# Kernel optimization log

Hardware: AMD Instinct MI355X
Metric: run time of the kernel (lower is better)

Reference implementation:

```python
import jax, jax.numpy as jnp
import numpy as np

N_NODES = 40000
N_EDGES = 640000
NFEAT = 256
NHID = 128


def setup_inputs() -> dict:
    key = jax.random.key(0)
    k1, k2, k3, k4 = jax.random.split(key, 4)
    x = jax.random.normal(k1, (N_NODES, NFEAT), dtype=jnp.float32)
    edge_index = jax.random.randint(k2, (2, N_EDGES), 0, N_NODES, dtype=jnp.int64)
    edge_weight = jax.random.uniform(k3, (N_EDGES,), dtype=jnp.float32)
    # Glorot-style init for the GraphConvolution weight, zero bias
    W = jax.random.normal(k4, (NFEAT, NHID), dtype=jnp.float32) * (1.0 / np.sqrt(NFEAT))
    b = jnp.zeros((NHID,), dtype=jnp.float32)
    return {"x": x, "edge_index": edge_index, "edge_weight": edge_weight, "W": W, "b": b}


def reference(x, edge_index, edge_weight, W, b):
    # GraphConvolution: support = x @ W ; out = spmm(adj, support) + b ; relu
    support = x @ W                                   # [N, nhid]
    src, dst = edge_index[0], edge_index[1]
    msgs = support[src] * edge_weight[:, None]        # [E, nhid] gathered messages
    agg = jax.ops.segment_sum(msgs, dst, num_segments=N_NODES)  # [N, nhid]
    return jax.nn.relu(agg + b)
```

## Files before the change

### kernel.cpp

```cpp
#include <hip/hip_runtime.h>

#define NNODES 40000
#define NEDGES 640000
#define NFEAT  256
#define NHID   128

#define RSHIFT 7
#define RNODES 128
#define NR     313
#define CAPR   3000
#define PARTB  250
#define EPT    10
#define EPB    2560
#define CAPB   32
#define GEMM_BLOCKS (NNODES / 64)

#define SUP_OFF  0u
#define WT_OFF   10240000u
#define CNT_OFF  10305536u
#define EBIN_OFF 10465536u
#define WS_NEEDED (EBIN_OFF + (size_t)NR * PARTB * CAPB * 8)

typedef float floatx4 __attribute__((ext_vector_type(4)));
typedef __bf16 bf16x8 __attribute__((ext_vector_type(8)));
typedef unsigned short ushort8 __attribute__((ext_vector_type(8)));
union BfFrag { ushort8 s; bf16x8 b; };

__device__ __forceinline__ unsigned short f2bf(float f) {
    unsigned int u = __float_as_uint(f);
    u = (u + 0x7FFFu + ((u >> 16) & 1u)) >> 16;
    return (unsigned short)u;
}

__device__ __forceinline__ float4 bf4(unsigned int lo, unsigned int hi) {
    float4 v;
    v.x = __uint_as_float(lo << 16);
    v.y = __uint_as_float(lo & 0xFFFF0000u);
    v.z = __uint_as_float(hi << 16);
    v.w = __uint_as_float(hi & 0xFFFF0000u);
    return v;
}

__global__ __launch_bounds__(256) void setup_wt(const float* __restrict__ W,
                                                unsigned short* __restrict__ Wt) {
    const int i = blockIdx.x * 256 + threadIdx.x;
    const int h = i >> 8;
    const int k = i & 255;
    Wt[i] = f2bf(W[k * NHID + h]);
}

__global__ __launch_bounds__(256) void gemm_fill(const float* __restrict__ x,
                                                 const unsigned short* __restrict__ Wt,
                                                 unsigned short* __restrict__ support,
                                                 const int* __restrict__ ei,
                                                 const float* __restrict__ ew,
                                                 unsigned short* __restrict__ cnt,
                                                 unsigned long long* __restrict__ ebin) {
    const int tid = threadIdx.x;

    if (blockIdx.x >= GEMM_BLOCKS) {
        __shared__ unsigned int ldscur[320];
        const int pb   = blockIdx.x - GEMM_BLOCKS;
        const int base = pb * EPB + tid;

        for (int i = tid; i < 320; i += 256) ldscur[i] = 0u;
        __syncthreads();

        int src[EPT], dst[EPT];
        float w[EPT];
        #pragma unroll
        for (int j = 0; j < EPT; j++) {
            const int e = base + j * 256;
            src[j] = ei[e];
            dst[j] = ei[NEDGES + e];
            w[j]   = ew[e];
        }
        #pragma unroll
        for (int j = 0; j < EPT; j++) {
            const int r = dst[j] >> RSHIFT;
            const unsigned int idx = atomicAdd(&ldscur[r], 1u);
            if (idx < CAPB) {
                const unsigned long long rec =
                    ((unsigned long long)f2bf(w[j]) << 32)
                  | ((unsigned long long)(dst[j] & (RNODES - 1)) << 16)
                  | (unsigned long long)(unsigned int)src[j];
                ebin[((size_t)r * PARTB + pb) * CAPB + idx] = rec;
            }
        }
        __syncthreads();

        for (int i = tid; i < NR; i += 256) {
            unsigned int c = ldscur[i];
            if (c > CAPB) c = CAPB;
            cnt[(size_t)pb * NR + i] = (unsigned short)c;
        }
        return;
    }

    const int lane = tid & 63;
    const int wv   = tid >> 6;
    const int m    = lane & 15;
    const int quad = lane >> 4;
    const int node = blockIdx.x * 64 + wv * 16 + m;

    BfFrag afrag[8];
    const float* xrow = x + (size_t)node * NFEAT + quad * 8;
    #pragma unroll
    for (int ks = 0; ks < 8; ks++) {
        float4 f0 = *(const float4*)(xrow + ks * 32);
        float4 f1 = *(const float4*)(xrow + ks * 32 + 4);
        afrag[ks].s[0] = f2bf(f0.x); afrag[ks].s[1] = f2bf(f0.y);
        afrag[ks].s[2] = f2bf(f0.z); afrag[ks].s[3] = f2bf(f0.w);
        afrag[ks].s[4] = f2bf(f1.x); afrag[ks].s[5] = f2bf(f1.y);
        afrag[ks].s[6] = f2bf(f1.z); afrag[ks].s[7] = f2bf(f1.w);
    }

    floatx4 acc[8];
    #pragma unroll
    for (int nt = 0; nt < 8; nt++) acc[nt] = (floatx4){0.f, 0.f, 0.f, 0.f};

    #pragma unroll
    for (int nt = 0; nt < 8; nt++) {
        const unsigned short* wrow = Wt + (size_t)(nt * 16 + m) * NFEAT + quad * 8;
        #pragma unroll
        for (int ks = 0; ks < 8; ks++) {
            BfFrag bfrag;
            bfrag.s = *(const ushort8*)(wrow + ks * 32);
            acc[nt] = __builtin_amdgcn_mfma_f32_16x16x32_bf16(afrag[ks].b, bfrag.b,
                                                              acc[nt], 0, 0, 0);
        }
    }

    const int row0 = blockIdx.x * 64 + wv * 16 + quad * 4;
    #pragma unroll
    for (int nt = 0; nt < 8; nt++) {
        #pragma unroll
        for (int r = 0; r < 4; r++) {
            support[(size_t)(row0 + r) * NHID + nt * 16 + m] = f2bf(acc[nt][r]);
        }
    }
}

__global__ __launch_bounds__(512) void gather_range(
        const unsigned short* __restrict__ cnt,
        const unsigned long long* __restrict__ ebin,
        const unsigned short* __restrict__ support,
        const float* __restrict__ b,
        float* __restrict__ out) {
    __shared__ unsigned long long srec[CAPR];
    __shared__ unsigned int hcnt[RNODES];
    __shared__ unsigned int hstart[RNODES + 1];
    __shared__ unsigned int sA[RNODES], sB[RNODES];

    const int r   = blockIdx.x;
    const int tid = threadIdx.x;

    unsigned int c_t = 0;
    const unsigned long long* seg =
        ebin + ((size_t)r * PARTB + (tid < PARTB ? tid : 0)) * CAPB;
    if (tid < PARTB) {
        c_t = cnt[(size_t)tid * NR + r];
        if (c_t > CAPB) c_t = CAPB;
    }
    if (tid < RNODES) hcnt[tid] = 0u;
    __syncthreads();

    for (unsigned int k = 0; k < c_t; ++k)
        atomicAdd(&hcnt[(unsigned int)(seg[k] >> 16) & (RNODES - 1)], 1u);
    __syncthreads();

    if (tid < RNODES) sA[tid] = (tid > 0) ? hcnt[tid - 1] : 0u;
    __syncthreads();
    unsigned int* cur = sA;
    unsigned int* nxt = sB;
    for (int off = 1; off < RNODES; off <<= 1) {
        if (tid < RNODES) nxt[tid] = cur[tid] + ((tid >= off) ? cur[tid - off] : 0u);
        __syncthreads();
        unsigned int* t = cur; cur = nxt; nxt = t;
    }
    if (tid < RNODES) hstart[tid] = cur[tid];
    if (tid == RNODES - 1) hstart[RNODES] = cur[RNODES - 1] + hcnt[RNODES - 1];
    __syncthreads();
    if (tid < RNODES) hcnt[tid] = hstart[tid];
    __syncthreads();

    for (unsigned int k = 0; k < c_t; ++k) {
        const unsigned long long rec = seg[k];
        const unsigned int dl = (unsigned int)(rec >> 16) & (RNODES - 1);
        const unsigned int p  = atomicAdd(&hcnt[dl], 1u);
        if (p < CAPR) srec[p] = rec;
    }
    __syncthreads();

    const int nl = tid >> 2;
    const int j  = tid & 3;
    unsigned int kb = hstart[nl];
    unsigned int ke = hstart[nl + 1];
    if (kb > CAPR) kb = CAPR;
    if (ke > CAPR) ke = CAPR;

    float acc[32];
    #pragma unroll
    for (int t = 0; t < 32; t++) acc[t] = 0.f;

    const uint4* sup4 = (const uint4*)support;
    #pragma unroll 2
    for (unsigned int k = kb; k < ke; ++k) {
        const unsigned long long rec = srec[k];
        const float w  = __uint_as_float(((unsigned int)(rec >> 32)) << 16);
        const int   sc = (int)(rec & 0xFFFFu);
        const uint4* rowp = sup4 + (size_t)sc * 16 + (j << 2);
        const uint4 u0 = rowp[0];
        const uint4 u1 = rowp[1];
        const uint4 u2 = rowp[2];
        const uint4 u3 = rowp[3];
        float4 v;
        v = bf4(u0.x, u0.y); acc[0] += w*v.x;  acc[1] += w*v.y;  acc[2] += w*v.z;  acc[3] += w*v.w;
        v = bf4(u0.z, u0.w); acc[4] += w*v.x;  acc[5] += w*v.y;  acc[6] += w*v.z;  acc[7] += w*v.w;
        v = bf4(u1.x, u1.y); acc[8] += w*v.x;  acc[9] += w*v.y;  acc[10] += w*v.z; acc[11] += w*v.w;
        v = bf4(u1.z, u1.w); acc[12] += w*v.x; acc[13] += w*v.y; acc[14] += w*v.z; acc[15] += w*v.w;
        v = bf4(u2.x, u2.y); acc[16] += w*v.x; acc[17] += w*v.y; acc[18] += w*v.z; acc[19] += w*v.w;
        v = bf4(u2.z, u2.w); acc[20] += w*v.x; acc[21] += w*v.y; acc[22] += w*v.z; acc[23] += w*v.w;
        v = bf4(u3.x, u3.y); acc[24] += w*v.x; acc[25] += w*v.y; acc[26] += w*v.z; acc[27] += w*v.w;
        v = bf4(u3.z, u3.w); acc[28] += w*v.x; acc[29] += w*v.y; acc[30] += w*v.z; acc[31] += w*v.w;
    }

    const int node = r * RNODES + nl;
    if (node < NNODES) {
        const float4* b4p = (const float4*)b + (j << 3);
        float4*       o4  = (float4*)out + (size_t)node * (NHID / 4) + (j << 3);
        #pragma unroll
        for (int t = 0; t < 8; t++) {
            float4 bb = b4p[t];
            float4 v;
            v.x = fmaxf(acc[t * 4 + 0] + bb.x, 0.f);
            v.y = fmaxf(acc[t * 4 + 1] + bb.y, 0.f);
            v.z = fmaxf(acc[t * 4 + 2] + bb.z, 0.f);
            v.w = fmaxf(acc[t * 4 + 3] + bb.w, 0.f);
            o4[t] = v;
        }
    }
}

__global__ __launch_bounds__(256) void gemm_xw(const float* __restrict__ x,
                                               const float* __restrict__ W,
                                               float* __restrict__ support) {
    __shared__ float xs[64 * NFEAT];
    const int tid   = threadIdx.x;
    const int node0 = blockIdx.x * 64;

    const float4* xg  = (const float4*)(x + (size_t)node0 * NFEAT);
    float4*       xs4 = (float4*)xs;
    #pragma unroll
    for (int i = tid; i < 64 * (NFEAT / 4); i += 256) xs4[i] = xg[i];
    __syncthreads();

    const int hg = tid & 31;
    const int ng = tid >> 5;
    const float4* W4 = (const float4*)W;

    float4 acc[8];
    #pragma unroll
    for (int n = 0; n < 8; n++) acc[n] = make_float4(0.f, 0.f, 0.f, 0.f);

    #pragma unroll 4
    for (int k = 0; k < NFEAT; k++) {
        float4 w = W4[k * (NHID / 4) + hg];
        #pragma unroll
        for (int n = 0; n < 8; n++) {
            float xv = xs[(ng * 8 + n) * NFEAT + k];
            acc[n].x = fmaf(xv, w.x, acc[n].x);
            acc[n].y = fmaf(xv, w.y, acc[n].y);
            acc[n].z = fmaf(xv, w.z, acc[n].z);
            acc[n].w = fmaf(xv, w.w, acc[n].w);
        }
    }

    float4* out4 = (float4*)support;
    #pragma unroll
    for (int n = 0; n < 8; n++)
        out4[(size_t)(node0 + ng * 8 + n) * (NHID / 4) + hg] = acc[n];
}

__global__ __launch_bounds__(256) void scatter_edges(const int* __restrict__ ei,
                                                     const float* __restrict__ ew,
                                                     const float* __restrict__ support,
                                                     float* __restrict__ out) {
    const int tid  = threadIdx.x;
    const int lane = tid & 31;
    const int e    = blockIdx.x * 8 + (tid >> 5);
    const int   src = ei[e];
    const int   dst = ei[NEDGES + e];
    const float w   = ew[e];
    const float4* s4 = (const float4*)support;
    float4 v = s4[(size_t)src * (NHID / 4) + lane];
    float* o = out + (size_t)dst * NHID + lane * 4;
    atomicAdd(o + 0, v.x * w);
    atomicAdd(o + 1, v.y * w);
    atomicAdd(o + 2, v.z * w);
    atomicAdd(o + 3, v.w * w);
}

__global__ __launch_bounds__(256) void finalize(float* __restrict__ out,
                                                const float* __restrict__ b) {
    const int i = blockIdx.x * 256 + threadIdx.x;
    float4*       o4 = (float4*)out;
    const float4* b4 = (const float4*)b;
    float4 v  = o4[i];
    float4 bb = b4[i & 31];
    v.x = fmaxf(v.x + bb.x, 0.f);
    v.y = fmaxf(v.y + bb.y, 0.f);
    v.z = fmaxf(v.z + bb.z, 0.f);
    v.w = fmaxf(v.w + bb.w, 0.f);
    o4[i] = v;
}

extern "C" void kernel_launch(void* const* d_in, const int* in_sizes, int n_in,
                              void* d_out, int out_size, void* d_ws, size_t ws_size,
                              hipStream_t stream) {
    const float* x  = (const float*)d_in[0];
    const int*   ei = (const int*)d_in[1];
    const float* ew = (const float*)d_in[2];
    const float* W  = (const float*)d_in[3];
    const float* b  = (const float*)d_in[4];
    float*       out = (float*)d_out;

    char* ws = (char*)d_ws;

    if (ws_size >= WS_NEEDED) {
        unsigned short*     support = (unsigned short*)(ws + SUP_OFF);
        unsigned short*     Wt      = (unsigned short*)(ws + WT_OFF);
        unsigned short*     cnt     = (unsigned short*)(ws + CNT_OFF);
        unsigned long long* ebin    = (unsigned long long*)(ws + EBIN_OFF);

        setup_wt<<<128, 256, 0, stream>>>(W, Wt);
        gemm_fill<<<GEMM_BLOCKS + PARTB, 256, 0, stream>>>(
            x, Wt, support, ei, ew, cnt, ebin);
        gather_range<<<NR, 512, 0, stream>>>(cnt, ebin, support, b, out);
    } else {
        float* support = (float*)(ws + SUP_OFF);
        gemm_xw<<<NNODES / 64, 256, 0, stream>>>(x, W, support);
        hipMemsetAsync(d_out, 0, (size_t)out_size * sizeof(float), stream);
        scatter_edges<<<NEDGES / 8, 256, 0, stream>>>(ei, ew, support, out);
        finalize<<<out_size / 4 / 256, 256, 0, stream>>>(out, b);
    }
}
```

Before: 156.5 us.

## Split each gather range across four blocks with 16 threads per node

The gather kernel now launches four blocks per 128-node range. Each block handles 32 destination nodes, filtering the binned edge records to its quarter, and assigns 16 threads per node, each loading one 16-byte chunk of the support row. This raises the block count from 313 to 1252 and cuts per-thread accumulator registers from 32 floats to 8, so occupancy and latency hiding should improve. In exchange, every block rereads and filters the full bin list for its range, quadrupling that scan and its atomics, and the per-block record capacity shrinks to 1024.

```diff
diff --git a/kernel.cpp b/kernel.cpp
--- a/kernel.cpp
+++ b/kernel.cpp
@@ -8,12 +8,14 @@
 #define RSHIFT 7
 #define RNODES 128
 #define NR     313
-#define CAPR   3000
 #define PARTB  250
 #define EPT    10
 #define EPB    2560
 #define CAPB   32
 #define GEMM_BLOCKS (NNODES / 64)
+#define WSPLIT 4
+#define WNODES 32
+#define CAPW   1024
 
 #define SUP_OFF  0u
 #define WT_OFF   10240000u
@@ -147,12 +149,13 @@
         const unsigned short* __restrict__ support,
         const float* __restrict__ b,
         float* __restrict__ out) {
-    __shared__ unsigned long long srec[CAPR];
-    __shared__ unsigned int hcnt[RNODES];
-    __shared__ unsigned int hstart[RNODES + 1];
-    __shared__ unsigned int sA[RNODES], sB[RNODES];
-
-    const int r   = blockIdx.x;
+    __shared__ unsigned long long srec[CAPW];
+    __shared__ unsigned int hcnt[WNODES];
+    __shared__ unsigned int hstart[WNODES + 1];
+    __shared__ unsigned int sA[WNODES], sB[WNODES];
+
+    const int r   = blockIdx.x >> 2;
+    const int q   = blockIdx.x & 3;
     const int tid = threadIdx.x;
 
     unsigned int c_t = 0;
@@ -162,83 +165,75 @@
         c_t = cnt[(size_t)tid * NR + r];
         if (c_t > CAPB) c_t = CAPB;
     }
-    if (tid < RNODES) hcnt[tid] = 0u;
-    __syncthreads();
-
-    for (unsigned int k = 0; k < c_t; ++k)
-        atomicAdd(&hcnt[(unsigned int)(seg[k] >> 16) & (RNODES - 1)], 1u);
-    __syncthreads();
-
-    if (tid < RNODES) sA[tid] = (tid > 0) ? hcnt[tid - 1] : 0u;
+    if (tid < WNODES) hcnt[tid] = 0u;
+    __syncthreads();
+
+    for (unsigned int k = 0; k < c_t; ++k) {
+        const unsigned int dl = (unsigned int)(seg[k] >> 16) & (RNODES - 1);
+        if ((int)(dl >> 5) == q) atomicAdd(&hcnt[dl & (WNODES - 1)], 1u);
+    }
+    __syncthreads();
+
+    if (tid < WNODES) sA[tid] = (tid > 0) ? hcnt[tid - 1] : 0u;
     __syncthreads();
     unsigned int* cur = sA;
     unsigned int* nxt = sB;
-    for (int off = 1; off < RNODES; off <<= 1) {
-        if (tid < RNODES) nxt[tid] = cur[tid] + ((tid >= off) ? cur[tid - off] : 0u);
+    for (int off = 1; off < WNODES; off <<= 1) {
+        if (tid < WNODES) nxt[tid] = cur[tid] + ((tid >= off) ? cur[tid - off] : 0u);
         __syncthreads();
         unsigned int* t = cur; cur = nxt; nxt = t;
     }
-    if (tid < RNODES) hstart[tid] = cur[tid];
-    if (tid == RNODES - 1) hstart[RNODES] = cur[RNODES - 1] + hcnt[RNODES - 1];
-    __syncthreads();
-    if (tid < RNODES) hcnt[tid] = hstart[tid];
+    if (tid < WNODES) hstart[tid] = cur[tid];
+    if (tid == WNODES - 1) hstart[WNODES] = cur[WNODES - 1] + hcnt[WNODES - 1];
+    __syncthreads();
+    if (tid < WNODES) hcnt[tid] = hstart[tid];
     __syncthreads();
 
     for (unsigned int k = 0; k < c_t; ++k) {
         const unsigned long long rec = seg[k];
         const unsigned int dl = (unsigned int)(rec >> 16) & (RNODES - 1);
-        const unsigned int p  = atomicAdd(&hcnt[dl], 1u);
-        if (p < CAPR) srec[p] = rec;
-    }
-    __syncthreads();
-
-    const int nl = tid >> 2;
-    const int j  = tid & 3;
+        if ((int)(dl >> 5) == q) {
+            const unsigned int p = atomicAdd(&hcnt[dl & (WNODES - 1)], 1u);
+            if (p < CAPW) srec[p] = rec;
+        }
+    }
+    __syncthreads();
+
+    const int nl = tid >> 4;
+    const int ql = tid & 15;
     unsigned int kb = hstart[nl];
     unsigned int ke = hstart[nl + 1];
-    if (kb > CAPR) kb = CAPR;
-    if (ke > CAPR) ke = CAPR;
-
-    float acc[32];
-    #pragma unroll
-    for (int t = 0; t < 32; t++) acc[t] = 0.f;
-
+    if (kb > CAPW) kb = CAPW;
+    if (ke > CAPW) ke = CAPW;
+
+    float4 lo = make_float4(0.f, 0.f, 0.f, 0.f);
+    float4 hi = lo;
     const uint4* sup4 = (const uint4*)support;
+
     #pragma unroll 2
     for (unsigned int k = kb; k < ke; ++k) {
         const unsigned long long rec = srec[k];
         const float w  = __uint_as_float(((unsigned int)(rec >> 32)) << 16);
         const int   sc = (int)(rec & 0xFFFFu);
-        const uint4* rowp = sup4 + (size_t)sc * 16 + (j << 2);
-        const uint4 u0 = rowp[0];
-        const uint4 u1 = rowp[1];
-        const uint4 u2 = rowp[2];
-        const uint4 u3 = rowp[3];
-        float4 v;
-        v = bf4(u0.x, u0.y); acc[0] += w*v.x;  acc[1] += w*v.y;  acc[2] += w*v.z;  acc[3] += w*v.w;
-        v = bf4(u0.z, u0.w); acc[4] += w*v.x;  acc[5] += w*v.y;  acc[6] += w*v.z;  acc[7] += w*v.w;
-        v = bf4(u1.x, u1.y); acc[8] += w*v.x;  acc[9] += w*v.y;  acc[10] += w*v.z; acc[11] += w*v.w;
-        v = bf4(u1.z, u1.w); acc[12] += w*v.x; acc[13] += w*v.y; acc[14] += w*v.z; acc[15] += w*v.w;
-        v = bf4(u2.x, u2.y); acc[16] += w*v.x; acc[17] += w*v.y; acc[18] += w*v.z; acc[19] += w*v.w;
-        v = bf4(u2.z, u2.w); acc[20] += w*v.x; acc[21] += w*v.y; acc[22] += w*v.z; acc[23] += w*v.w;
-        v = bf4(u3.x, u3.y); acc[24] += w*v.x; acc[25] += w*v.y; acc[26] += w*v.z; acc[27] += w*v.w;
-        v = bf4(u3.z, u3.w); acc[28] += w*v.x; acc[29] += w*v.y; acc[30] += w*v.z; acc[31] += w*v.w;
-    }
-
-    const int node = r * RNODES + nl;
+        const uint4 u  = sup4[(size_t)sc * 16 + ql];
+        const float4 vl = bf4(u.x, u.y), vh = bf4(u.z, u.w);
+        lo.x = fmaf(w, vl.x, lo.x); lo.y = fmaf(w, vl.y, lo.y);
+        lo.z = fmaf(w, vl.z, lo.z); lo.w = fmaf(w, vl.w, lo.w);
+        hi.x = fmaf(w, vh.x, hi.x); hi.y = fmaf(w, vh.y, hi.y);
+        hi.z = fmaf(w, vh.z, hi.z); hi.w = fmaf(w, vh.w, hi.w);
+    }
+
+    const int node = r * RNODES + q * WNODES + nl;
     if (node < NNODES) {
-        const float4* b4p = (const float4*)b + (j << 3);
-        float4*       o4  = (float4*)out + (size_t)node * (NHID / 4) + (j << 3);
-        #pragma unroll
-        for (int t = 0; t < 8; t++) {
-            float4 bb = b4p[t];
-            float4 v;
-            v.x = fmaxf(acc[t * 4 + 0] + bb.x, 0.f);
-            v.y = fmaxf(acc[t * 4 + 1] + bb.y, 0.f);
-            v.z = fmaxf(acc[t * 4 + 2] + bb.z, 0.f);
-            v.w = fmaxf(acc[t * 4 + 3] + bb.w, 0.f);
-            o4[t] = v;
-        }
+        const float4* b4p = (const float4*)b;
+        float4 bl = b4p[ql * 2], bh = b4p[ql * 2 + 1];
+        lo.x = fmaxf(lo.x + bl.x, 0.f); lo.y = fmaxf(lo.y + bl.y, 0.f);
+        lo.z = fmaxf(lo.z + bl.z, 0.f); lo.w = fmaxf(lo.w + bl.w, 0.f);
+        hi.x = fmaxf(hi.x + bh.x, 0.f); hi.y = fmaxf(hi.y + bh.y, 0.f);
+        hi.z = fmaxf(hi.z + bh.z, 0.f); hi.w = fmaxf(hi.w + bh.w, 0.f);
+        float4* o4 = (float4*)out + (size_t)node * (NHID / 4);
+        o4[ql * 2]     = lo;
+        o4[ql * 2 + 1] = hi;
     }
 }
 
@@ -336,7 +331,7 @@
         setup_wt<<<128, 256, 0, stream>>>(W, Wt);
         gemm_fill<<<GEMM_BLOCKS + PARTB, 256, 0, stream>>>(
             x, Wt, support, ei, ew, cnt, ebin);
-        gather_range<<<NR, 512, 0, stream>>>(cnt, ebin, support, b, out);
+        gather_range<<<NR * WSPLIT, 512, 0, stream>>>(cnt, ebin, support, b, out);
     } else {
         float* support = (float*)(ws + SUP_OFF);
         gemm_xw<<<NNODES / 64, 256, 0, stream>>>(x, W, support);
```

Result: slower. 168.0 us (+7.3%).
